# Optimization experiments

Hardware: AMD Instinct MI355X
Metric: run time of the kernel (lower is better)

The kernel has to match this reference:

```python
import jax, jax.numpy as jnp
import numpy as np

B, C, HS, WS = 2, 256, 64, 64
HF, WF = 128, 128
NH = 8
HD = C // NH
K, S, P = 3, 2, 1


def unfold_k3_s2_p1(x):
    # torch nn.Unfold((3,3), stride=2, padding=1): output [B, C*9, L], channel-major
    # ordering idx = c*9 + kh*3 + kw, L row-major over output positions.
    b, c, h, w = x.shape
    xp = jnp.pad(x, ((0, 0), (0, 0), (P, P), (P, P)))
    ho = (h + 2 * P - K) // S + 1
    wo = (w + 2 * P - K) // S + 1
    parts = [xp[:, :, kh:kh + S * (ho - 1) + 1:S, kw:kw + S * (wo - 1) + 1:S]
             for kh in range(K) for kw in range(K)]
    patches = jnp.stack(parts, axis=2)  # [B, C, 9, ho, wo]
    return patches.reshape(b, c * K * K, ho * wo)


def setup_inputs() -> dict:
    key = jax.random.key(0)
    ks = jax.random.split(key, 7)
    w_scale = jnp.float32(0.02)
    return {
        "feat": jax.random.normal(ks[0], (B, C, HF, WF), dtype=jnp.float32),
        "src": jax.random.normal(ks[1], (B, C, HS, WS), dtype=jnp.float32),
        "Wq": jax.random.normal(ks[2], (C, C), dtype=jnp.float32) * w_scale,
        "bq": jnp.zeros((C,), dtype=jnp.float32),
        "Wk": jax.random.normal(ks[3], (C, C), dtype=jnp.float32) * w_scale,
        "bk": jnp.zeros((C,), dtype=jnp.float32),
        "Wv": jax.random.normal(ks[4], (C, C), dtype=jnp.float32) * w_scale,
        "bv": jnp.zeros((C,), dtype=jnp.float32),
        "Wo": jax.random.normal(ks[5], (C, C), dtype=jnp.float32) * w_scale,
        "bo": jnp.zeros((C,), dtype=jnp.float32),
    }


def reference(feat, src, Wq, bq, Wk, bk, Wv, bv, Wo, bo):
    b, c, h, w = src.shape
    # query: 1x1 unfold == flatten spatial -> [B, Lq, C]
    query = src.reshape(b, c, h * w).transpose(0, 2, 1)
    # key/value: 3x3 im2col of feat, then keep only FIRST c entries of the C*9 dim
    kv = unfold_k3_s2_p1(feat).transpose(0, 2, 1)[..., :c]  # [B, Lkv, C]
    # MultiheadAttention (batch_first), embed_dim=C, 8 heads
    q = query @ Wq.T + bq
    k = kv @ Wk.T + bk
    v = kv @ Wv.T + bv

    def split_heads(x):
        return x.reshape(b, -1, NH, HD).transpose(0, 2, 1, 3)  # [B, H, L, D]

    qh, kh_, vh = split_heads(q), split_heads(k), split_heads(v)
    scale = jnp.float32(1.0 / np.sqrt(HD))
    scores = jnp.einsum('bhqd,bhkd->bhqk', qh, kh_) * scale
    attn = jax.nn.softmax(scores, axis=-1)
    oh = jnp.einsum('bhqk,bhkd->bhqd', attn, vh)
    o = oh.transpose(0, 2, 1, 3).reshape(b, -1, c)
    o = o @ Wo.T + bo  # out projection
    # fold with kernel (1,1) == reshape back to [B, C, h, w]
    out = o.transpose(0, 2, 1).reshape(b, c, h, w)
    return out * src
```

## Files before the change

### kernel.cpp

```cpp
#include <hip/hip_runtime.h>
#include <math.h>

#define B_  2
#define C_  256
#define NH_ 8
#define HD_ 32
#define L_  4096
#define M_  (B_*L_)

typedef __attribute__((ext_vector_type(8))) short bf16x8;
typedef __attribute__((ext_vector_type(4))) float f32x4;

__device__ __forceinline__ unsigned short f2bf(float x) {
    unsigned u = __float_as_uint(x);
    unsigned r = u + 0x7fffu + ((u >> 16) & 1u);
    return (unsigned short)(r >> 16);
}

#define GLOAD_LDS16(gp, lp) \
    __builtin_amdgcn_global_load_lds( \
        (const __attribute__((address_space(1))) void*)(gp), \
        (__attribute__((address_space(3))) void*)(lp), 16, 0, 0)

__global__ __launch_bounds__(256) void build_kv_kernel(
    const float* __restrict__ feat, float* __restrict__ kv)
{
    int idx = blockIdx.x * 256 + threadIdx.x;
    int j = idx & (C_ - 1);
    int l = (idx >> 8) & (L_ - 1);
    int b = idx >> 20;
    int c  = j / 9;
    int r  = j - c * 9;
    int kh = r / 3;
    int kw = r - kh * 3;
    int oh = l >> 6, ow = l & 63;
    int h = 2 * oh + kh - 1;
    int w = 2 * ow + kw - 1;
    float val = 0.0f;
    if ((unsigned)h < 128u && (unsigned)w < 128u)
        val = feat[((size_t)(b * C_ + c) * 128 + h) * 128 + w];
    kv[idx] = val;
}

template <bool TRANS_A, int OMODE>
__global__ __launch_bounds__(256) void gemm_kernel(
    const float* __restrict__ A, const float* __restrict__ W,
    const float* __restrict__ bias, void* __restrict__ out,
    const float* __restrict__ src, float oscale)
{
    __shared__ float As[32][68];
    __shared__ float Ws[32][68];

    const int m0 = blockIdx.x * 64;
    const int n0 = blockIdx.y * 64;
    const int t  = threadIdx.x;
    const int tm = t >> 4;
    const int tn = t & 15;

    float acc[4][4] = {};

    for (int k0 = 0; k0 < C_; k0 += 32) {
        if (!TRANS_A) {
            #pragma unroll
            for (int u = t; u < 512; u += 256) {
                int row = u >> 3, c4 = u & 7;
                float4 val = *(const float4*)(A + (size_t)(m0 + row) * C_ + k0 + c4 * 4);
                As[c4 * 4 + 0][row] = val.x;
                As[c4 * 4 + 1][row] = val.y;
                As[c4 * 4 + 2][row] = val.z;
                As[c4 * 4 + 3][row] = val.w;
            }
        } else {
            int b  = m0 >> 12;
            int l0 = m0 & (L_ - 1);
            #pragma unroll
            for (int u = t; u < 512; u += 256) {
                int c = u >> 4, l4 = u & 15;
                float4 val = *(const float4*)(A + (size_t)b * C_ * L_ +
                                              (size_t)(k0 + c) * L_ + l0 + l4 * 4);
                *(float4*)&As[c][l4 * 4] = val;
            }
        }
        #pragma unroll
        for (int u = t; u < 512; u += 256) {
            int row = u >> 3, c4 = u & 7;
            float4 val = *(const float4*)(W + (size_t)(n0 + row) * C_ + k0 + c4 * 4);
            Ws[c4 * 4 + 0][row] = val.x;
            Ws[c4 * 4 + 1][row] = val.y;
            Ws[c4 * 4 + 2][row] = val.z;
            Ws[c4 * 4 + 3][row] = val.w;
        }
        __syncthreads();
        #pragma unroll
        for (int kk = 0; kk < 32; kk++) {
            float4 a4 = *(float4*)&As[kk][tm * 4];
            float4 w4 = *(float4*)&Ws[kk][tn * 4];
            float a[4] = {a4.x, a4.y, a4.z, a4.w};
            float w[4] = {w4.x, w4.y, w4.z, w4.w};
            #pragma unroll
            for (int i = 0; i < 4; i++)
                #pragma unroll
                for (int jj = 0; jj < 4; jj++)
                    acc[i][jj] += a[i] * w[jj];
        }
        __syncthreads();
    }

    if (OMODE == 1) {
        unsigned short* o = (unsigned short*)out;
        #pragma unroll
        for (int i = 0; i < 4; i++) {
            int m = m0 + tm * 4 + i;
            int n = n0 + tn * 4;
            ushort4 pk = make_ushort4(
                f2bf((acc[i][0] + bias[n + 0]) * oscale),
                f2bf((acc[i][1] + bias[n + 1]) * oscale),
                f2bf((acc[i][2] + bias[n + 2]) * oscale),
                f2bf((acc[i][3] + bias[n + 3]) * oscale));
            *(ushort4*)(o + ((size_t)m << 8) + n) = pk;
        }
    } else if (OMODE == 2) {
        unsigned short* o = (unsigned short*)out;
        int b = m0 >> 12;
        int key = (m0 & (L_ - 1)) + tm * 4;
        #pragma unroll
        for (int jj = 0; jj < 4; jj++) {
            int n = n0 + tn * 4 + jj;
            float bb = bias[n];
            ushort4 pk = make_ushort4(
                f2bf(acc[0][jj] + bb), f2bf(acc[1][jj] + bb),
                f2bf(acc[2][jj] + bb), f2bf(acc[3][jj] + bb));
            *(ushort4*)(o + ((size_t)(b * 256 + n) << 12) + key) = pk;
        }
    } else {
        float* o = (float*)out;
        #pragma unroll
        for (int i = 0; i < 4; i++) {
            int m = m0 + tm * 4 + i;
            int b = m >> 12, l = m & (L_ - 1);
            #pragma unroll
            for (int jj = 0; jj < 4; jj++) {
                int n = n0 + tn * 4 + jj;
                float val = acc[i][jj] + bias[n];
                size_t oidx = (size_t)(b * C_ + n) * L_ + l;
                o[oidx] = val * src[oidx];
            }
        }
    }
}

__global__ __launch_bounds__(512) void attn_mfma_kernel(
    const unsigned short* __restrict__ qbf,
    const unsigned short* __restrict__ kbf,
    const unsigned short* __restrict__ vbf,
    float* __restrict__ ob)
{
    __shared__ __align__(16) char Ksh[2][4096];
    __shared__ __align__(16) char Vsh[2][4096];
    __shared__ float mb[4][64][11];

    const int id   = blockIdx.x;
    const int xcd  = id & 7;
    const int slot = id >> 3;
    const int bh   = xcd + 8 * (slot >> 6);
    const int qt   = slot & 63;
    const int b = bh >> 3, h = bh & 7;

    const int t      = threadIdx.x;
    const int lane   = t & 63;
    const int wl     = (t >> 6) & 3;
    const int halfid = t >> 8;
    const int th     = t & 255;
    const int lg     = lane >> 4;
    const int lc     = lane & 15;

    const int qrow = qt * 64 + wl * 16 + lc;
    const bf16x8 qf = *(const bf16x8*)(qbf + ((size_t)(b * L_ + qrow) << 8) + h * 32 + (lg << 3));

    const char* kg = (const char*)kbf
        + ((size_t)(b * L_ + halfid * 2048 + wl * 16 + lc) << 9) + h * 64 + (lg << 4);
    const int vmt = (t >> 7) & 1, vks = wl & 1;
    const char* vg = (const char*)vbf
        + ((size_t)(b * 256 + h * 32 + vmt * 16 + lc) << 13)
        + ((size_t)(halfid * 2048 + vks * 32 + (lg << 3)) << 1);
    char* kdst = Ksh[halfid] + th * 16;
    char* vdst = Vsh[halfid] + th * 16;
    const char* kbase = Ksh[halfid];
    const char* vbase = Vsh[halfid];

    f32x4 oacc[2];
    oacc[0] = (f32x4){0.f, 0.f, 0.f, 0.f};
    oacc[1] = (f32x4){0.f, 0.f, 0.f, 0.f};
    float mrun = -INFINITY, lrun = 0.0f;
    const f32x4 zero4 = (f32x4){0.f, 0.f, 0.f, 0.f};

    for (int kt = 0; kt < 32; kt++) {
        __syncthreads();
        GLOAD_LDS16(kg + (size_t)kt * 32768, kdst);
        GLOAD_LDS16(vg + (size_t)kt * 128,   vdst);
        __syncthreads();

        f32x4 sa[4];
        #pragma unroll
        for (int f = 0; f < 4; f++) {
            bf16x8 kf = *(const bf16x8*)(kbase + f * 1024 + lane * 16);
            sa[f] = __builtin_amdgcn_mfma_f32_16x16x32_bf16(kf, qf, zero4, 0, 0, 0);
        }

        float sv[16];
        #pragma unroll
        for (int f = 0; f < 4; f++)
            #pragma unroll
            for (int i = 0; i < 4; i++)
                sv[f * 4 + i] = sa[f][i];
        float t0 = fmaxf(fmaxf(sv[0], sv[1]),  fmaxf(sv[2], sv[3]));
        float t1 = fmaxf(fmaxf(sv[4], sv[5]),  fmaxf(sv[6], sv[7]));
        float t2 = fmaxf(fmaxf(sv[8], sv[9]),  fmaxf(sv[10], sv[11]));
        float t3 = fmaxf(fmaxf(sv[12], sv[13]), fmaxf(sv[14], sv[15]));
        float tmax = fmaxf(fmaxf(t0, t1), fmaxf(t2, t3));
        tmax = fmaxf(tmax, __shfl_xor(tmax, 16));
        tmax = fmaxf(tmax, __shfl_xor(tmax, 32));
        float mnew   = fmaxf(mrun, tmax);
        float factor = exp2f(mrun - mnew);
        float pv[16];
        float ps = 0.f;
        #pragma unroll
        for (int j2 = 0; j2 < 16; j2++) {
            float p = exp2f(sv[j2] - mnew);
            pv[j2] = p;
            ps += p;
        }
        ps += __shfl_xor(ps, 16);
        ps += __shfl_xor(ps, 32);
        lrun = lrun * factor + ps;
        mrun = mnew;
        #pragma unroll
        for (int i = 0; i < 4; i++) { oacc[0][i] *= factor; oacc[1][i] *= factor; }

        unsigned W8[8];
        #pragma unroll
        for (int f = 0; f < 4; f++)
            #pragma unroll
            for (int m2 = 0; m2 < 2; m2++)
                W8[f * 2 + m2] = (unsigned)f2bf(pv[f * 4 + 2 * m2])
                               | ((unsigned)f2bf(pv[f * 4 + 2 * m2 + 1]) << 16);

        #pragma unroll
        for (int ks = 0; ks < 2; ks++) {
            union { unsigned u[4]; bf16x8 v; } bu;
            #pragma unroll
            for (int j = 0; j < 4; j++) {
                int srcl = lc + 16 * ((lg & 1) * 2 + (j >> 1));
                unsigned va = (unsigned)__shfl((int)W8[(ks * 2) * 2 + (j & 1)], srcl);
                unsigned vb = (unsigned)__shfl((int)W8[(ks * 2 + 1) * 2 + (j & 1)], srcl);
                bu.u[j] = (lg >= 2) ? vb : va;
            }
            bf16x8 v0 = *(const bf16x8*)(vbase + 0 * 2048 + ks * 1024 + lane * 16);
            bf16x8 v1 = *(const bf16x8*)(vbase + 1 * 2048 + ks * 1024 + lane * 16);
            oacc[0] = __builtin_amdgcn_mfma_f32_16x16x32_bf16(v0, bu.v, oacc[0], 0, 0, 0);
            oacc[1] = __builtin_amdgcn_mfma_f32_16x16x32_bf16(v1, bu.v, oacc[1], 0, 0, 0);
        }
    }

    __syncthreads();
    if (halfid == 1) {
        float* s = &mb[wl][lane][0];
        #pragma unroll
        for (int i = 0; i < 4; i++) { s[i] = oacc[0][i]; s[4 + i] = oacc[1][i]; }
        s[8] = mrun; s[9] = lrun;
    }
    __syncthreads();
    if (halfid == 0) {
        const float* s = &mb[wl][lane][0];
        float m1 = s[8], l1 = s[9];
        float mF = fmaxf(mrun, m1);
        float f0 = exp2f(mrun - mF);
        float f1 = exp2f(m1 - mF);
        float invl = 1.0f / (lrun * f0 + l1 * f1);
        #pragma unroll
        for (int mt = 0; mt < 2; mt++) {
            f32x4 ov;
            #pragma unroll
            for (int i = 0; i < 4; i++)
                ov[i] = (oacc[mt][i] * f0 + s[mt * 4 + i] * f1) * invl;
            *(f32x4*)(ob + ((size_t)(b * L_ + qrow) << 8) + h * 32 + mt * 16 + (lg << 2)) = ov;
        }
    }
}

extern "C" void kernel_launch(void* const* d_in, const int* in_sizes, int n_in,
                              void* d_out, int out_size, void* d_ws, size_t ws_size,
                              hipStream_t stream)
{
    const float* feat = (const float*)d_in[0];
    const float* src  = (const float*)d_in[1];
    const float* Wq   = (const float*)d_in[2];
    const float* bq   = (const float*)d_in[3];
    const float* Wk   = (const float*)d_in[4];
    const float* bk   = (const float*)d_in[5];
    const float* Wv   = (const float*)d_in[6];
    const float* bv   = (const float*)d_in[7];
    const float* Wo   = (const float*)d_in[8];
    const float* bo   = (const float*)d_in[9];
    float* out = (float*)d_out;

    float* ws = (float*)d_ws;
    const size_t NE = (size_t)M_ * C_;
    float* kv = ws;
    float* ob = ws + NE;
    unsigned short* qbf = (unsigned short*)(ws + 2 * NE);
    unsigned short* kbf = qbf + NE;
    unsigned short* vbf = kbf + NE;

    build_kv_kernel<<<(B_ * L_ * C_) / 256, 256, 0, stream>>>(feat, kv);

    const float qscale = 0.17677669529663687f * 1.4426950408889634f;

    dim3 ggrid(M_ / 64, C_ / 64);
    gemm_kernel<true,  1><<<ggrid, 256, 0, stream>>>(src, Wq, bq, qbf, nullptr, qscale);
    gemm_kernel<false, 1><<<ggrid, 256, 0, stream>>>(kv,  Wk, bk, kbf, nullptr, 1.0f);
    gemm_kernel<false, 2><<<ggrid, 256, 0, stream>>>(kv,  Wv, bv, vbf, nullptr, 1.0f);

    attn_mfma_kernel<<<1024, 512, 0, stream>>>(qbf, kbf, vbf, ob);

    gemm_kernel<false, 3><<<ggrid, 256, 0, stream>>>(ob, Wo, bo, out, src, 1.0f);
}
```

Baseline: 320.7 us.

## Move Q/K/V projections to bf16 MFMA GEMMs with pre-cast inputs

The Q, K and V projections now run as bf16 MFMA GEMMs in place of the fp32 FMA GEMMs. Each block loads the whole K=256 slab into swizzled LDS with global_load_lds. To feed them, the kv im2col is written directly as bf16, src is transposed and cast to bf16 by a new kernel, and the three weight matrices are cast to bf16. This targets the scalar-FMA compute and fp32 traffic of the projections. In exchange it adds two small extra launches and lowers precision of the projection inputs. The output projection stays on the fp32 path.

```diff
diff --git a/kernel.cpp b/kernel.cpp
--- a/kernel.cpp
+++ b/kernel.cpp
@@ -3,8 +3,6 @@
 
 #define B_  2
 #define C_  256
-#define NH_ 8
-#define HD_ 32
 #define L_  4096
 #define M_  (B_*L_)
 
@@ -23,7 +21,7 @@
         (__attribute__((address_space(3))) void*)(lp), 16, 0, 0)
 
 __global__ __launch_bounds__(256) void build_kv_kernel(
-    const float* __restrict__ feat, float* __restrict__ kv)
+    const float* __restrict__ feat, unsigned short* __restrict__ kvbf)
 {
     int idx = blockIdx.x * 256 + threadIdx.x;
     int j = idx & (C_ - 1);
@@ -39,14 +37,134 @@
     float val = 0.0f;
     if ((unsigned)h < 128u && (unsigned)w < 128u)
         val = feat[((size_t)(b * C_ + c) * 128 + h) * 128 + w];
-    kv[idx] = val;
-}
-
-template <bool TRANS_A, int OMODE>
-__global__ __launch_bounds__(256) void gemm_kernel(
+    kvbf[idx] = f2bf(val);
+}
+
+__global__ __launch_bounds__(256) void transpose_cast_kernel(
+    const float* __restrict__ src, unsigned short* __restrict__ srcT)
+{
+    __shared__ float T[64][68];
+    const int id = blockIdx.x;
+    const int b  = id >> 8;
+    const int rem = id & 255;
+    const int c0 = (rem >> 6) << 6;
+    const int l0 = (rem & 63) << 6;
+    const int t = threadIdx.x;
+    const int tc = t >> 2, tl = (t & 3) * 16;
+    const float* srow = src + ((size_t)(b * C_ + c0 + tc) << 12) + l0 + tl;
+    #pragma unroll
+    for (int i = 0; i < 4; i++)
+        *(float4*)&T[tc][tl + i * 4] = *(const float4*)(srow + i * 4);
+    __syncthreads();
+    const int tl2 = t >> 2, tcc = (t & 3) * 16;
+    unsigned short* orow = srcT + ((size_t)(b * L_ + l0 + tl2) << 8) + c0 + tcc;
+    union { bf16x8 v; unsigned short s[8]; } p0, p1;
+    #pragma unroll
+    for (int j = 0; j < 8; j++) p0.s[j] = f2bf(T[tcc + j][tl2]);
+    #pragma unroll
+    for (int j = 0; j < 8; j++) p1.s[j] = f2bf(T[tcc + 8 + j][tl2]);
+    *(bf16x8*)orow = p0.v;
+    *(bf16x8*)(orow + 8) = p1.v;
+}
+
+__global__ __launch_bounds__(256) void cast_w_kernel(
+    const float* __restrict__ Wq, const float* __restrict__ Wk,
+    const float* __restrict__ Wv, unsigned short* __restrict__ wb)
+{
+    int t = blockIdx.x * 256 + threadIdx.x;
+    int mi = t >> 14;
+    int e4 = (t & 16383) * 4;
+    const float* W = (mi == 0) ? Wq : (mi == 1) ? Wk : Wv;
+    float4 v = *(const float4*)(W + e4);
+    ushort4 pk = make_ushort4(f2bf(v.x), f2bf(v.y), f2bf(v.z), f2bf(v.w));
+    *(ushort4*)(wb + mi * 65536 + e4) = pk;
+}
+
+template <int VOUT>
+__global__ __launch_bounds__(256) void proj_gemm_kernel(
+    const unsigned short* __restrict__ A, const unsigned short* __restrict__ Wb,
+    const float* __restrict__ bias, unsigned short* __restrict__ out, float oscale)
+{
+    __shared__ __align__(16) char Ash[32768];
+    __shared__ __align__(16) char Wsh[32768];
+    const int m0 = blockIdx.x * 64;
+    const int n0 = blockIdx.y * 64;
+    const int t = threadIdx.x;
+
+    #pragma unroll
+    for (int i = 0; i < 8; i++) {
+        int off = t * 16 + i * 4096;
+        int rl = off >> 9;
+        int sw = (off & 511) ^ ((rl & 7) << 4);
+        GLOAD_LDS16((const char*)A  + (((size_t)(m0 + rl)) << 9) + sw, Ash + off);
+        GLOAD_LDS16((const char*)Wb + (((size_t)(n0 + rl)) << 9) + sw, Wsh + off);
+    }
+    __syncthreads();
+
+    const int lane = t & 63, w = t >> 6;
+    const int lg = lane >> 4, lc = lane & 15;
+    const int wm = w & 1, wn = w >> 1;
+
+    f32x4 acc[2][2];
+    #pragma unroll
+    for (int i = 0; i < 2; i++)
+        #pragma unroll
+        for (int j = 0; j < 2; j++)
+            acc[i][j] = (f32x4){0.f, 0.f, 0.f, 0.f};
+
+    #pragma unroll
+    for (int ks = 0; ks < 8; ks++) {
+        bf16x8 af[2], wf[2];
+        #pragma unroll
+        for (int g = 0; g < 2; g++) {
+            int ra = wm * 32 + g * 16 + lc;
+            af[g] = *(const bf16x8*)(Ash + ra * 512 + ((ks * 64 + lg * 16) ^ ((ra & 7) << 4)));
+            int rw = wn * 32 + g * 16 + lc;
+            wf[g] = *(const bf16x8*)(Wsh + rw * 512 + ((ks * 64 + lg * 16) ^ ((rw & 7) << 4)));
+        }
+        #pragma unroll
+        for (int mg = 0; mg < 2; mg++)
+            #pragma unroll
+            for (int ng = 0; ng < 2; ng++)
+                acc[mg][ng] = VOUT
+                    ? __builtin_amdgcn_mfma_f32_16x16x32_bf16(wf[ng], af[mg], acc[mg][ng], 0, 0, 0)
+                    : __builtin_amdgcn_mfma_f32_16x16x32_bf16(af[mg], wf[ng], acc[mg][ng], 0, 0, 0);
+    }
+
+    if (VOUT == 0) {
+        #pragma unroll
+        for (int mg = 0; mg < 2; mg++) {
+            int m = m0 + wm * 32 + mg * 16 + lg * 4;
+            #pragma unroll
+            for (int ng = 0; ng < 2; ng++) {
+                int n = n0 + wn * 32 + ng * 16 + lc;
+                float bb = bias[n];
+                #pragma unroll
+                for (int i = 0; i < 4; i++)
+                    out[(size_t)(m + i) * 256 + n] = f2bf((acc[mg][ng][i] + bb) * oscale);
+            }
+        }
+    } else {
+        int b = m0 >> 12, key = m0 & (L_ - 1);
+        #pragma unroll
+        for (int ng = 0; ng < 2; ng++)
+            #pragma unroll
+            for (int i = 0; i < 4; i++) {
+                int n = n0 + wn * 32 + ng * 16 + lg * 4 + i;
+                float bb = bias[n];
+                #pragma unroll
+                for (int mg = 0; mg < 2; mg++) {
+                    int m = key + wm * 32 + mg * 16 + lc;
+                    out[((size_t)(b * 256 + n) << 12) + m] = f2bf(acc[mg][ng][i] + bb);
+                }
+            }
+    }
+}
+
+__global__ __launch_bounds__(256) void o_proj_kernel(
     const float* __restrict__ A, const float* __restrict__ W,
-    const float* __restrict__ bias, void* __restrict__ out,
-    const float* __restrict__ src, float oscale)
+    const float* __restrict__ bias, float* __restrict__ out,
+    const float* __restrict__ src)
 {
     __shared__ float As[32][68];
     __shared__ float Ws[32][68];
@@ -60,26 +178,14 @@
     float acc[4][4] = {};
 
     for (int k0 = 0; k0 < C_; k0 += 32) {
-        if (!TRANS_A) {
-            #pragma unroll
-            for (int u = t; u < 512; u += 256) {
-                int row = u >> 3, c4 = u & 7;
-                float4 val = *(const float4*)(A + (size_t)(m0 + row) * C_ + k0 + c4 * 4);
-                As[c4 * 4 + 0][row] = val.x;
-                As[c4 * 4 + 1][row] = val.y;
-                As[c4 * 4 + 2][row] = val.z;
-                As[c4 * 4 + 3][row] = val.w;
-            }
-        } else {
-            int b  = m0 >> 12;
-            int l0 = m0 & (L_ - 1);
-            #pragma unroll
-            for (int u = t; u < 512; u += 256) {
-                int c = u >> 4, l4 = u & 15;
-                float4 val = *(const float4*)(A + (size_t)b * C_ * L_ +
-                                              (size_t)(k0 + c) * L_ + l0 + l4 * 4);
-                *(float4*)&As[c][l4 * 4] = val;
-            }
+        #pragma unroll
+        for (int u = t; u < 512; u += 256) {
+            int row = u >> 3, c4 = u & 7;
+            float4 val = *(const float4*)(A + (size_t)(m0 + row) * C_ + k0 + c4 * 4);
+            As[c4 * 4 + 0][row] = val.x;
+            As[c4 * 4 + 1][row] = val.y;
+            As[c4 * 4 + 2][row] = val.z;
+            As[c4 * 4 + 3][row] = val.w;
         }
         #pragma unroll
         for (int u = t; u < 512; u += 256) {
@@ -96,55 +202,26 @@
             float4 a4 = *(float4*)&As[kk][tm * 4];
             float4 w4 = *(float4*)&Ws[kk][tn * 4];
             float a[4] = {a4.x, a4.y, a4.z, a4.w};
-            float w[4] = {w4.x, w4.y, w4.z, w4.w};
+            float wv[4] = {w4.x, w4.y, w4.z, w4.w};
             #pragma unroll
             for (int i = 0; i < 4; i++)
                 #pragma unroll
                 for (int jj = 0; jj < 4; jj++)
-                    acc[i][jj] += a[i] * w[jj];
+                    acc[i][jj] += a[i] * wv[jj];
         }
         __syncthreads();
     }
 
-    if (OMODE == 1) {
-        unsigned short* o = (unsigned short*)out;
-        #pragma unroll
-        for (int i = 0; i < 4; i++) {
-            int m = m0 + tm * 4 + i;
-            int n = n0 + tn * 4;
-            ushort4 pk = make_ushort4(
-                f2bf((acc[i][0] + bias[n + 0]) * oscale),
-                f2bf((acc[i][1] + bias[n + 1]) * oscale),
-                f2bf((acc[i][2] + bias[n + 2]) * oscale),
-                f2bf((acc[i][3] + bias[n + 3]) * oscale));
-            *(ushort4*)(o + ((size_t)m << 8) + n) = pk;
-        }
-    } else if (OMODE == 2) {
-        unsigned short* o = (unsigned short*)out;
-        int b = m0 >> 12;
-        int key = (m0 & (L_ - 1)) + tm * 4;
+    #pragma unroll
+    for (int i = 0; i < 4; i++) {
+        int m = m0 + tm * 4 + i;
+        int b = m >> 12, l = m & (L_ - 1);
         #pragma unroll
         for (int jj = 0; jj < 4; jj++) {
             int n = n0 + tn * 4 + jj;
-            float bb = bias[n];
-            ushort4 pk = make_ushort4(
-                f2bf(acc[0][jj] + bb), f2bf(acc[1][jj] + bb),
-                f2bf(acc[2][jj] + bb), f2bf(acc[3][jj] + bb));
-            *(ushort4*)(o + ((size_t)(b * 256 + n) << 12) + key) = pk;
-        }
-    } else {
-        float* o = (float*)out;
-        #pragma unroll
-        for (int i = 0; i < 4; i++) {
-            int m = m0 + tm * 4 + i;
-            int b = m >> 12, l = m & (L_ - 1);
-            #pragma unroll
-            for (int jj = 0; jj < 4; jj++) {
-                int n = n0 + tn * 4 + jj;
-                float val = acc[i][jj] + bias[n];
-                size_t oidx = (size_t)(b * C_ + n) * L_ + l;
-                o[oidx] = val * src[oidx];
-            }
+            float val = acc[i][jj] + bias[n];
+            size_t oidx = (size_t)(b * C_ + n) * L_ + l;
+            out[oidx] = val * src[oidx];
         }
     }
 }
@@ -306,22 +383,26 @@
 
     float* ws = (float*)d_ws;
     const size_t NE = (size_t)M_ * C_;
-    float* kv = ws;
-    float* ob = ws + NE;
-    unsigned short* qbf = (unsigned short*)(ws + 2 * NE);
-    unsigned short* kbf = qbf + NE;
-    unsigned short* vbf = kbf + NE;
-
-    build_kv_kernel<<<(B_ * L_ * C_) / 256, 256, 0, stream>>>(feat, kv);
+    float* ob = ws;
+    unsigned short* qbf  = (unsigned short*)(ws + NE);
+    unsigned short* kbf  = qbf + NE;
+    unsigned short* vbf  = kbf + NE;
+    unsigned short* kvbf = vbf + NE;
+    unsigned short* srcT = kvbf + NE;
+    unsigned short* wb   = srcT + NE;
 
     const float qscale = 0.17677669529663687f * 1.4426950408889634f;
 
-    dim3 ggrid(M_ / 64, C_ / 64);
-    gemm_kernel<true,  1><<<ggrid, 256, 0, stream>>>(src, Wq, bq, qbf, nullptr, qscale);
-    gemm_kernel<false, 1><<<ggrid, 256, 0, stream>>>(kv,  Wk, bk, kbf, nullptr, 1.0f);
-    gemm_kernel<false, 2><<<ggrid, 256, 0, stream>>>(kv,  Wv, bv, vbf, nullptr, 1.0f);
+    build_kv_kernel<<<(B_ * L_ * C_) / 256, 256, 0, stream>>>(feat, kvbf);
+    transpose_cast_kernel<<<512, 256, 0, stream>>>(src, srcT);
+    cast_w_kernel<<<192, 256, 0, stream>>>(Wq, Wk, Wv, wb);
+
+    dim3 pgrid(M_ / 64, C_ / 64);
+    proj_gemm_kernel<0><<<pgrid, 256, 0, stream>>>(srcT, wb,          bq, qbf, qscale);
+    proj_gemm_kernel<0><<<pgrid, 256, 0, stream>>>(kvbf, wb + 65536,  bk, kbf, 1.0f);
+    proj_gemm_kernel<1><<<pgrid, 256, 0, stream>>>(kvbf, wb + 131072, bv, vbf, 1.0f);
 
     attn_mfma_kernel<<<1024, 512, 0, stream>>>(qbf, kbf, vbf, ob);
 
-    gemm_kernel<false, 3><<<ggrid, 256, 0, stream>>>(ob, Wo, bo, out, src, 1.0f);
-}
+    o_proj_kernel<<<pgrid, 256, 0, stream>>>(ob, Wo, bo, out, src);
+}
```

Result: faster. 274.1 us (-14.5%).
